# Performance work log

Measured on AMD Instinct MI355X. Metric: run time of the kernel, lower is better.

Reference implementation:

```python
import jax, jax.numpy as jnp
import numpy as np

BATCH, H, N, L = 8, 1024, 64, 4096

def setup_inputs() -> dict:
    key = jax.random.key(0)
    k1, k2, k3, k4, k5 = jax.random.split(key, 5)
    du = jax.random.normal(k1, (BATCH, H, L), dtype=jnp.float32)
    C = jax.random.normal(k2, (H, N), dtype=jnp.float32)
    Bvec = jax.random.normal(k3, (N,), dtype=jnp.float32)
    A = jax.random.normal(k4, (N, N), dtype=jnp.float32)
    W = jax.random.normal(k5, (N, H), dtype=jnp.float32)  # 'nh' projection from forward's randn(H,N) under subscript nh
    return {"du": du, "C": C, "Bvec": Bvec, "A": A, "W": W}

def reference(du, C, Bvec, A, W):
    # deltaA[b,n,l] = sum_h du[b,h,l] * W[n,h]
    deltaA = jnp.einsum('bhl,nh->bnl', du, W)            # (B, N, L)
    # A_t = A + diag(S_t), S_t = prefix-sum of deltaA over time
    S = jnp.cumsum(deltaA, axis=-1)                      # (B, N, L)
    # K[b,h,t] = C[h,:] @ (A_t[b] @ Bvec)
    #          = C @ (A @ Bvec)  +  (C * Bvec) @ S[b,:,t]
    base = C @ (A @ Bvec)                                # (H,)
    K = base[None, :, None] + jnp.einsum('hn,bnl->bhl', C * Bvec[None, :], S)
    return K  # (B, H, L)
```

## Files before the change

### kernel.cpp

```cpp
#include <hip/hip_runtime.h>
#include <hip/hip_bf16.h>

#define B_ 8
#define H_ 1024
#define N_ 64
#define L_ 4096

typedef float f32x4 __attribute__((ext_vector_type(4)));
typedef int   i32x4 __attribute__((ext_vector_type(4)));

__device__ __forceinline__ unsigned bfpk(float a, float b) {
    unsigned ua = (unsigned)__builtin_bit_cast(unsigned short, __float2bfloat16(a));
    unsigned ub = (unsigned)__builtin_bit_cast(unsigned short, __float2bfloat16(b));
    return ua | (ub << 16);
}

__device__ __forceinline__ void mfma16(f32x4& d, i32x4 a, i32x4 b) {
    asm volatile("s_nop 1\n\tv_mfma_f32_16x16x32_bf16 %0, %1, %2, %0"
                 : "+v"(d) : "v"(a), "v"(b));
}

__global__ __launch_bounds__(256) void setup_kernel(
    const float* __restrict__ C, const float* __restrict__ Bvec,
    const float* __restrict__ A, const float* __restrict__ W,
    unsigned short* __restrict__ Wswz, unsigned short* __restrict__ CBswz,
    float* __restrict__ base)
{
    const int tid = threadIdx.x, bid = blockIdx.x;
    const int lane = tid & 63, lm = lane & 15, lq = lane >> 4;
    if (bid < 32) {
        const int kt = bid, nt = tid >> 6;
        const float* src = W + (size_t)(nt * 16 + lm) * H_ + kt * 32 + lq * 8;
        float4 a = *(const float4*)src, c = *(const float4*)(src + 4);
        i32x4 o;
        o.x = bfpk(a.x, a.y); o.y = bfpk(a.z, a.w);
        o.z = bfpk(c.x, c.y); o.w = bfpk(c.z, c.w);
        ((i32x4*)Wswz)[(kt * 4 + nt) * 64 + lane] = o;
    } else if (bid < 64) {
        const int u = (bid - 32) * 4 + (tid >> 6);
        const int mt = u & 63, kt = u >> 6;
        const int h = mt * 16 + lm, n0 = kt * 32 + lq * 8;
        const float* src = C + (size_t)h * 64 + n0;
        float4 a = *(const float4*)src, c = *(const float4*)(src + 4);
        float4 v1 = *(const float4*)(Bvec + n0), v2 = *(const float4*)(Bvec + n0 + 4);
        i32x4 o;
        o.x = bfpk(a.x * v1.x, a.y * v1.y); o.y = bfpk(a.z * v1.z, a.w * v1.w);
        o.z = bfpk(c.x * v2.x, c.y * v2.y); o.w = bfpk(c.z * v2.z, c.w * v2.w);
        ((i32x4*)CBswz)[u * 64 + lane] = o;
    } else {
        __shared__ float abv[64];
        __shared__ float bv[64];
        if (tid < 64) bv[tid] = Bvec[tid];
        __syncthreads();
        if (tid < 64) {
            float s = 0.f;
            const float* ar = A + tid * 64;
            #pragma unroll 8
            for (int m = 0; m < 64; ++m) s += ar[m] * bv[m];
            abv[tid] = s;
        }
        __syncthreads();
        #pragma unroll
        for (int r = 0; r < 4; ++r) {
            int h = tid + r * 256;
            float s = 0.f;
            const float* cr = C + (size_t)h * 64;
            #pragma unroll 8
            for (int n = 0; n < 64; ++n) s += cr[n] * abv[n];
            base[h] = s;
        }
    }
}

__global__ __launch_bounds__(512) void dA_kernel(
    const float* __restrict__ du, const unsigned short* __restrict__ Wswz,
    float* __restrict__ dAf, float* __restrict__ Tsum)
{
    __shared__ float red[4][64][16];
    const int tid = threadIdx.x, lane = tid & 63, w = tid >> 6;
    const int st = w & 3, half = w >> 2;
    const int lt = blockIdx.x, b = blockIdx.y;
    const int lm = lane & 15, lq = lane >> 4;
    const int myl = lt * 64 + st * 16 + lm;
    const float* dup = du + ((size_t)b * H_ + (size_t)half * 512) * L_ + myl;

    f32x4 acc[4] = {f32x4{0,0,0,0}, f32x4{0,0,0,0}, f32x4{0,0,0,0}, f32x4{0,0,0,0}};
    #pragma unroll 4
    for (int kt = 0; kt < 16; ++kt) {
        const int h0 = kt * 32 + lq * 8;
        float d[8];
        #pragma unroll
        for (int j = 0; j < 8; ++j) d[j] = dup[(size_t)(h0 + j) * L_];
        i32x4 af;
        af.x = bfpk(d[0], d[1]); af.y = bfpk(d[2], d[3]);
        af.z = bfpk(d[4], d[5]); af.w = bfpk(d[6], d[7]);
        const int ktg = half * 16 + kt;
        #pragma unroll
        for (int nt = 0; nt < 4; ++nt) {
            i32x4 bfr = ((const i32x4*)Wswz)[(ktg * 4 + nt) * 64 + lane];
            mfma16(acc[nt], af, bfr);
        }
    }
    asm volatile("s_nop 7\n\ts_nop 7"
                 : "+v"(acc[0]), "+v"(acc[1]), "+v"(acc[2]), "+v"(acc[3]));

    if (half == 1) {
        #pragma unroll
        for (int nt = 0; nt < 4; ++nt)
            #pragma unroll
            for (int r = 0; r < 4; ++r)
                red[st][lane][nt * 4 + r] = acc[nt][r];
    }
    __syncthreads();
    if (half == 1) return;

    #pragma unroll
    for (int nt = 0; nt < 4; ++nt)
        #pragma unroll
        for (int r = 0; r < 4; ++r)
            acc[nt][r] += red[st][lane][nt * 4 + r];

    float* outp = dAf + ((size_t)b * L_ + (size_t)lt * 64 + st * 16 + lq * 4) * 64 + lm;
    #pragma unroll
    for (int nt = 0; nt < 4; ++nt) {
        #pragma unroll
        for (int r = 0; r < 4; ++r)
            outp[(size_t)r * 64 + nt * 16] = acc[nt][r];
    }
    float s[4];
    #pragma unroll
    for (int nt = 0; nt < 4; ++nt) {
        float v = acc[nt][0] + acc[nt][1] + acc[nt][2] + acc[nt][3];
        v += __shfl_xor(v, 16);
        v += __shfl_xor(v, 32);
        s[nt] = v;
    }
    float outv = (lq == 0) ? s[0] : (lq == 1) ? s[1] : (lq == 2) ? s[2] : s[3];
    Tsum[((size_t)b * 256 + lt * 4 + st) * 64 + lq * 16 + lm] = outv;
}

__global__ __launch_bounds__(512) void pscan_kernel(float* __restrict__ Tsum)
{
    const int tid = threadIdx.x, lane = tid & 63, w = tid >> 6;
    const int wid = blockIdx.x * 8 + w;
    const int b = wid >> 6, n = wid & 63;
    float* p = Tsum + (size_t)b * 256 * 64 + n;

    float v[4];
    #pragma unroll
    for (int j = 0; j < 4; ++j) v[j] = p[(size_t)(lane * 4 + j) * 64];
    float sum = v[0] + v[1] + v[2] + v[3];

    float sc = sum;
    #pragma unroll
    for (int d = 1; d < 64; d <<= 1) {
        float u = __shfl_up(sc, d);
        if (lane >= d) sc += u;
    }
    float run = sc - sum;
    #pragma unroll
    for (int j = 0; j < 4; ++j) {
        float t = v[j];
        p[(size_t)(lane * 4 + j) * 64] = run;
        run += t;
    }
}

__global__ __launch_bounds__(256) void out_kernel(
    const float* __restrict__ dAf, const float* __restrict__ Ppre,
    const unsigned short* __restrict__ CBswz, const float* __restrict__ base,
    float* __restrict__ K)
{
    __shared__ float slds[16][65];
    __shared__ float tot[4][64];
    const int tid = threadIdx.x;
    const int stile = blockIdx.x, b = blockIdx.y;
    const int l0 = stile * 16;
    {
        const int n = tid & 63, q = tid >> 6;
        const float* dp = dAf + ((size_t)b * L_ + l0 + q * 4) * 64 + n;
        float v0 = dp[0], v1 = dp[64], v2 = dp[128], v3 = dp[192];
        float s1 = v0 + v1, s2 = s1 + v2, s3 = s2 + v3;
        tot[q][n] = s3;
        __syncthreads();
        float off = Ppre[((size_t)b * 256 + stile) * 64 + n];
        if (q > 0) off += tot[0][n];
        if (q > 1) off += tot[1][n];
        if (q > 2) off += tot[2][n];
        slds[q * 4 + 0][n] = off + v0;
        slds[q * 4 + 1][n] = off + s1;
        slds[q * 4 + 2][n] = off + s2;
        slds[q * 4 + 3][n] = off + s3;
    }
    __syncthreads();

    const int lane = tid & 63, w = tid >> 6;
    const int lm = lane & 15, lq = lane >> 4;
    i32x4 sf[2];
    #pragma unroll
    for (int kt = 0; kt < 2; ++kt) {
        const float* sr = &slds[lm][kt * 32 + lq * 8];
        float x0 = sr[0], x1 = sr[1], x2 = sr[2], x3 = sr[3];
        float x4 = sr[4], x5 = sr[5], x6 = sr[6], x7 = sr[7];
        i32x4 t;
        t.x = bfpk(x0, x1); t.y = bfpk(x2, x3);
        t.z = bfpk(x4, x5); t.w = bfpk(x6, x7);
        sf[kt] = t;
    }

    f32x4 acc[16];
    #pragma unroll
    for (int i = 0; i < 16; ++i) {
        float4 bb = *(const float4*)(base + w * 256 + i * 16 + lq * 4);
        acc[i] = f32x4{bb.x, bb.y, bb.z, bb.w};
    }
    #pragma unroll
    for (int kt = 0; kt < 2; ++kt) {
        #pragma unroll
        for (int i = 0; i < 16; ++i) {
            i32x4 cb = ((const i32x4*)CBswz)[(kt * 64 + w * 16 + i) * 64 + lane];
            mfma16(acc[i], cb, sf[kt]);
        }
    }
    asm volatile("s_nop 7\n\ts_nop 7"
                 : "+v"(acc[0]), "+v"(acc[1]), "+v"(acc[2]), "+v"(acc[3]),
                   "+v"(acc[4]), "+v"(acc[5]), "+v"(acc[6]), "+v"(acc[7]),
                   "+v"(acc[8]), "+v"(acc[9]), "+v"(acc[10]), "+v"(acc[11]),
                   "+v"(acc[12]), "+v"(acc[13]), "+v"(acc[14]), "+v"(acc[15]));

    float* kp = K + ((size_t)b * H_ + w * 256 + lq * 4) * (size_t)L_ + l0 + lm;
    #pragma unroll
    for (int i = 0; i < 16; ++i) {
        #pragma unroll
        for (int r = 0; r < 4; ++r)
            kp[((size_t)i * 16 + r) * L_] = acc[i][r];
    }
}

extern "C" void kernel_launch(void* const* d_in, const int* in_sizes, int n_in,
                              void* d_out, int out_size, void* d_ws, size_t ws_size,
                              hipStream_t stream) {
    const float* du   = (const float*)d_in[0];
    const float* C    = (const float*)d_in[1];
    const float* Bvec = (const float*)d_in[2];
    const float* A    = (const float*)d_in[3];
    const float* W    = (const float*)d_in[4];
    float* K = (float*)d_out;

    float* dAf = (float*)d_ws;
    unsigned short* Wswz  = (unsigned short*)(dAf + (size_t)B_ * L_ * 64);
    unsigned short* CBswz = Wswz + 65536;
    float* Tsum = (float*)(CBswz + 65536);
    float* base = Tsum + (size_t)B_ * 256 * 64;

    setup_kernel<<<65, 256, 0, stream>>>(C, Bvec, A, W, Wswz, CBswz, base);
    dA_kernel<<<dim3(64, B_), 512, 0, stream>>>(du, Wswz, dAf, Tsum);
    pscan_kernel<<<64, 512, 0, stream>>>(Tsum);
    out_kernel<<<dim3(256, B_), 256, 0, stream>>>(dAf, Tsum, CBswz, base, K);
}
```

Before: 292.5 us.

## Retile output kernel to 64x256 tiles with LDS-staged coalesced float4 stores

Each out_kernel block now covers 64 time steps by 256 channels instead of 16 time steps by all 1024 channels. This lets each CB fragment load feed four MFMAs and cuts the per-block prefix recompute. Output stores go through LDS transposition so each row is written as contiguous float4 segments, replacing strided scalar stores. The base computation in setup is split across 4 blocks instead of one block looping. The cost is more LDS traffic, extra syncs, and a longer serial 16-step prefix per thread.

```diff
diff --git a/kernel.cpp b/kernel.cpp
--- a/kernel.cpp
+++ b/kernel.cpp
@@ -60,15 +60,12 @@
             abv[tid] = s;
         }
         __syncthreads();
-        #pragma unroll
-        for (int r = 0; r < 4; ++r) {
-            int h = tid + r * 256;
-            float s = 0.f;
-            const float* cr = C + (size_t)h * 64;
-            #pragma unroll 8
-            for (int n = 0; n < 64; ++n) s += cr[n] * abv[n];
-            base[h] = s;
-        }
+        const int h = (bid - 64) * 256 + tid;
+        float s = 0.f;
+        const float* cr = C + (size_t)h * 64;
+        #pragma unroll 8
+        for (int n = 0; n < 64; ++n) s += cr[n] * abv[n];
+        base[h] = s;
     }
 }
 
@@ -171,69 +168,86 @@
     const unsigned short* __restrict__ CBswz, const float* __restrict__ base,
     float* __restrict__ K)
 {
-    __shared__ float slds[16][65];
-    __shared__ float tot[4][64];
+    __shared__ float slds[64][65];
     const int tid = threadIdx.x;
-    const int stile = blockIdx.x, b = blockIdx.y;
-    const int l0 = stile * 16;
+    const int lt = blockIdx.x, hq = blockIdx.y, b = blockIdx.z;
+    const int l0 = lt * 64;
+
     {
         const int n = tid & 63, q = tid >> 6;
-        const float* dp = dAf + ((size_t)b * L_ + l0 + q * 4) * 64 + n;
-        float v0 = dp[0], v1 = dp[64], v2 = dp[128], v3 = dp[192];
-        float s1 = v0 + v1, s2 = s1 + v2, s3 = s2 + v3;
-        tot[q][n] = s3;
-        __syncthreads();
-        float off = Ppre[((size_t)b * 256 + stile) * 64 + n];
-        if (q > 0) off += tot[0][n];
-        if (q > 1) off += tot[1][n];
-        if (q > 2) off += tot[2][n];
-        slds[q * 4 + 0][n] = off + v0;
-        slds[q * 4 + 1][n] = off + s1;
-        slds[q * 4 + 2][n] = off + s2;
-        slds[q * 4 + 3][n] = off + s3;
+        const float* dp = dAf + ((size_t)b * L_ + l0 + q * 16) * 64 + n;
+        float run = Ppre[((size_t)b * 256 + lt * 4 + q) * 64 + n];
+        #pragma unroll
+        for (int r = 0; r < 16; ++r) {
+            run += dp[(size_t)r * 64];
+            slds[q * 16 + r][n] = run;
+        }
     }
     __syncthreads();
 
     const int lane = tid & 63, w = tid >> 6;
     const int lm = lane & 15, lq = lane >> 4;
-    i32x4 sf[2];
+
+    i32x4 sf[2][4];
     #pragma unroll
     for (int kt = 0; kt < 2; ++kt) {
-        const float* sr = &slds[lm][kt * 32 + lq * 8];
-        float x0 = sr[0], x1 = sr[1], x2 = sr[2], x3 = sr[3];
-        float x4 = sr[4], x5 = sr[5], x6 = sr[6], x7 = sr[7];
-        i32x4 t;
-        t.x = bfpk(x0, x1); t.y = bfpk(x2, x3);
-        t.z = bfpk(x4, x5); t.w = bfpk(x6, x7);
-        sf[kt] = t;
-    }
-
-    f32x4 acc[16];
-    #pragma unroll
-    for (int i = 0; i < 16; ++i) {
-        float4 bb = *(const float4*)(base + w * 256 + i * 16 + lq * 4);
-        acc[i] = f32x4{bb.x, bb.y, bb.z, bb.w};
+        #pragma unroll
+        for (int lt4 = 0; lt4 < 4; ++lt4) {
+            const float* sr = &slds[lt4 * 16 + lm][kt * 32 + lq * 8];
+            float x0 = sr[0], x1 = sr[1], x2 = sr[2], x3 = sr[3];
+            float x4 = sr[4], x5 = sr[5], x6 = sr[6], x7 = sr[7];
+            i32x4 t;
+            t.x = bfpk(x0, x1); t.y = bfpk(x2, x3);
+            t.z = bfpk(x4, x5); t.w = bfpk(x6, x7);
+            sf[kt][lt4] = t;
+        }
+    }
+
+    f32x4 acc[4][4];
+    #pragma unroll
+    for (int m = 0; m < 4; ++m) {
+        float4 bb = *(const float4*)(base + hq * 256 + w * 64 + m * 16 + lq * 4);
+        f32x4 bv = f32x4{bb.x, bb.y, bb.z, bb.w};
+        #pragma unroll
+        for (int lt4 = 0; lt4 < 4; ++lt4) acc[m][lt4] = bv;
     }
     #pragma unroll
     for (int kt = 0; kt < 2; ++kt) {
         #pragma unroll
-        for (int i = 0; i < 16; ++i) {
-            i32x4 cb = ((const i32x4*)CBswz)[(kt * 64 + w * 16 + i) * 64 + lane];
-            mfma16(acc[i], cb, sf[kt]);
+        for (int m = 0; m < 4; ++m) {
+            const int mtg = hq * 16 + w * 4 + m;
+            i32x4 cb = ((const i32x4*)CBswz)[(kt * 64 + mtg) * 64 + lane];
+            #pragma unroll
+            for (int lt4 = 0; lt4 < 4; ++lt4)
+                mfma16(acc[m][lt4], cb, sf[kt][lt4]);
         }
     }
     asm volatile("s_nop 7\n\ts_nop 7"
-                 : "+v"(acc[0]), "+v"(acc[1]), "+v"(acc[2]), "+v"(acc[3]),
-                   "+v"(acc[4]), "+v"(acc[5]), "+v"(acc[6]), "+v"(acc[7]),
-                   "+v"(acc[8]), "+v"(acc[9]), "+v"(acc[10]), "+v"(acc[11]),
-                   "+v"(acc[12]), "+v"(acc[13]), "+v"(acc[14]), "+v"(acc[15]));
-
-    float* kp = K + ((size_t)b * H_ + w * 256 + lq * 4) * (size_t)L_ + l0 + lm;
-    #pragma unroll
-    for (int i = 0; i < 16; ++i) {
-        #pragma unroll
-        for (int r = 0; r < 4; ++r)
-            kp[((size_t)i * 16 + r) * L_] = acc[i][r];
+                 : "+v"(acc[0][0]), "+v"(acc[0][1]), "+v"(acc[0][2]), "+v"(acc[0][3]),
+                   "+v"(acc[1][0]), "+v"(acc[1][1]), "+v"(acc[1][2]), "+v"(acc[1][3]),
+                   "+v"(acc[2][0]), "+v"(acc[2][1]), "+v"(acc[2][2]), "+v"(acc[2][3]),
+                   "+v"(acc[3][0]), "+v"(acc[3][1]), "+v"(acc[3][2]), "+v"(acc[3][3]));
+
+    __syncthreads();
+    const int row4 = lane >> 4;
+    const int seg  = lane & 15;
+    #pragma unroll
+    for (int m = 0; m < 4; ++m) {
+        #pragma unroll
+        for (int lt4 = 0; lt4 < 4; ++lt4)
+            #pragma unroll
+            for (int r = 0; r < 4; ++r)
+                slds[w * 16 + lq * 4 + r][lt4 * 16 + lm] = acc[m][lt4][r];
+        #pragma unroll
+        for (int r2 = 0; r2 < 4; ++r2) {
+            const int hl = r2 * 4 + row4;
+            const float* sp2 = &slds[w * 16 + hl][seg * 4];
+            float4 v;
+            v.x = sp2[0]; v.y = sp2[1]; v.z = sp2[2]; v.w = sp2[3];
+            float* kp = K + ((size_t)b * H_ + hq * 256 + w * 64 + m * 16 + hl) * (size_t)L_
+                          + l0 + seg * 4;
+            *(float4*)kp = v;
+        }
     }
 }
 
@@ -253,8 +267,8 @@
     float* Tsum = (float*)(CBswz + 65536);
     float* base = Tsum + (size_t)B_ * 256 * 64;
 
-    setup_kernel<<<65, 256, 0, stream>>>(C, Bvec, A, W, Wswz, CBswz, base);
+    setup_kernel<<<68, 256, 0, stream>>>(C, Bvec, A, W, Wswz, CBswz, base);
     dA_kernel<<<dim3(64, B_), 512, 0, stream>>>(du, Wswz, dAf, Tsum);
     pscan_kernel<<<64, 512, 0, stream>>>(Tsum);
-    out_kernel<<<dim3(256, B_), 256, 0, stream>>>(dAf, Tsum, CBswz, base, K);
-}
+    out_kernel<<<dim3(64, 4, B_), 256, 0, stream>>>(dAf, Tsum, CBswz, base, K);
+}
```

After: 276.5 us. 1.06x faster.
